# Optimization experiments

Hardware: AMD Instinct MI355X
Metric: run time of the kernel (lower is better)

Reference implementation:

```python
import jax, jax.numpy as jnp
import numpy as np

N_NODES = 100000
N_RAND_EDGES = 1200000
IN_DIM = 64
K = 10  # number of propagation hops


def setup_inputs() -> dict:
    key = jax.random.key(0)
    k1, k2, k3, k4 = jax.random.split(key, 4)
    feats = jax.random.normal(k1, (N_NODES, IN_DIM), dtype=jnp.float32)
    # xavier_uniform with sigmoid gain (=1.0) for s: bound = sqrt(6/(fan_in+fan_out))
    bound = float(np.sqrt(6.0 / (IN_DIM + 1)))
    s = jax.random.uniform(k2, (IN_DIM, 1), dtype=jnp.float32, minval=-bound, maxval=bound)
    src_r = jax.random.randint(k3, (N_RAND_EDGES,), 0, N_NODES)
    dst_r = jax.random.randint(k4, (N_RAND_EDGES,), 0, N_NODES)
    loops = jnp.arange(N_NODES)
    # append self-loops so every node has in_degree >= 1 (finite deg^-0.5)
    src = jnp.concatenate([src_r, loops]).astype(jnp.int64)
    dst = jnp.concatenate([dst_r, loops]).astype(jnp.int64)
    return {"feats": feats, "s": s, "src": src, "dst": dst}


def reference(feats, s, src, dst):
    n = feats.shape[0]
    ones = jnp.ones(src.shape[0], dtype=feats.dtype)
    degs = jax.ops.segment_sum(ones, dst, num_segments=n)  # in-degrees [N]
    norm = (degs ** -0.5)[:, None]  # [N,1]
    results = [feats]
    h = feats
    for _ in range(K):
        h = h * norm                                        # pre-scale
        h = jax.ops.segment_sum(h[src], dst, num_segments=n)  # copy_u + sum SpMM
        h = h * norm                                        # post-scale
        results.append(h)
    H = jnp.stack(results, axis=1)  # [N, K+1, D]
    S = jax.nn.sigmoid(jnp.einsum('nkd,do->nk', H, s))  # [N, K+1] gates
    return jnp.einsum('nk,nkd->nd', S, H)  # [N, D]
```

## Files before the change

### kernel.cpp

```cpp
#include <hip/hip_runtime.h>
#include <hip/hip_bf16.h>
#include <hip/hip_fp16.h>
#include <math.h>


#define DIM 64
#define BSH 9
#define BSZ 512
#define MAXNB 256
#define A2_CHUNK 4096
#define DBINS 64
#define DCHUNK 2048

__global__ void zero_int_kernel(int* __restrict__ p, int n) {
    int i = blockIdx.x * blockDim.x + threadIdx.x;
    if (i < n) p[i] = 0;
}

__global__ void bin_count_kernel(const int* __restrict__ dst,
                                 int* __restrict__ binCount, int E) {
    __shared__ int lb[MAXNB];
    if (threadIdx.x < MAXNB) lb[threadIdx.x] = 0;
    __syncthreads();
    for (int e = blockIdx.x * blockDim.x + threadIdx.x; e < E;
         e += gridDim.x * blockDim.x) {
        atomicAdd(&lb[dst[e] >> BSH], 1);
    }
    __syncthreads();
    if (threadIdx.x < MAXNB && lb[threadIdx.x])
        atomicAdd(&binCount[threadIdx.x], lb[threadIdx.x]);
}

__global__ void binscan_kernel(const int* __restrict__ binCount,
                               int* __restrict__ binBase, int* __restrict__ tail,
                               int* __restrict__ rp, int NB, int N, int E) {
    __shared__ int lds[256];
    int t = threadIdx.x;
    int v = (t < NB) ? binCount[t] : 0;
    lds[t] = v;
    __syncthreads();
    for (int off = 1; off < 256; off <<= 1) {
        int x = (t >= off) ? lds[t - off] : 0;
        __syncthreads();
        lds[t] += x;
        __syncthreads();
    }
    int excl = lds[t] - v;
    if (t < NB) { binBase[t] = excl; tail[t] = excl; }
    if (t == 0) { binBase[NB] = E; rp[N] = E; }
}

__global__ void bin_scatter_kernel(const int* __restrict__ src,
                                   const int* __restrict__ dst,
                                   int* __restrict__ tail,
                                   int2* __restrict__ pairs, int E) {
    __shared__ int cnt[MAXNB];
    __shared__ int base[MAXNB];
    int t = threadIdx.x;
    int begE = blockIdx.x * A2_CHUNK;
    int endE = begE + A2_CHUNK; if (endE > E) endE = E;
    if (t < MAXNB) cnt[t] = 0;
    __syncthreads();
    for (int e = begE + t; e < endE; e += blockDim.x)
        atomicAdd(&cnt[dst[e] >> BSH], 1);
    __syncthreads();
    if (t < MAXNB) {
        int c = cnt[t];
        base[t] = c ? atomicAdd(&tail[t], c) : 0;
        cnt[t] = 0;
    }
    __syncthreads();
    for (int e = begE + t; e < endE; e += blockDim.x) {
        int d = dst[e];
        int b = d >> BSH;
        int pos = base[b] + atomicAdd(&cnt[b], 1);
        pairs[pos] = make_int2(src[e], d);
    }
}

__global__ void bucket_build_kernel(const int2* __restrict__ pairs,
                                    const int* __restrict__ binBase,
                                    int* __restrict__ col, int* __restrict__ rp,
                                    float* __restrict__ norm, int N) {
    __shared__ int degL[BSZ];
    __shared__ int off[BSZ];
    __shared__ int tmp[256];
    int b  = blockIdx.x;
    int lo = b << BSH;
    int cnt = N - lo; if (cnt > BSZ) cnt = BSZ;
    int t = threadIdx.x;
    degL[t] = 0; degL[t + 256] = 0;
    __syncthreads();
    int rbeg = binBase[b], rend = binBase[b + 1];
    for (int j = rbeg + t; j < rend; j += 256)
        atomicAdd(&degL[pairs[j].y - lo], 1);
    __syncthreads();
    int d0 = degL[2 * t], d1 = degL[2 * t + 1];
    int s2 = d0 + d1;
    tmp[t] = s2;
    __syncthreads();
    for (int o = 1; o < 256; o <<= 1) {
        int x = (t >= o) ? tmp[t - o] : 0;
        __syncthreads();
        tmp[t] += x;
        __syncthreads();
    }
    int e2 = tmp[t] - s2;
    off[2 * t]     = e2;
    off[2 * t + 1] = e2 + d0;
    __syncthreads();
    if (2 * t < cnt) {
        rp[lo + 2 * t] = rbeg + e2;
        norm[lo + 2 * t] = rsqrtf((float)d0);
    }
    if (2 * t + 1 < cnt) {
        rp[lo + 2 * t + 1] = rbeg + e2 + d0;
        norm[lo + 2 * t + 1] = rsqrtf((float)d1);
    }
    for (int j = rbeg + t; j < rend; j += 256) {
        int2 p = pairs[j];
        int slot = atomicAdd(&off[p.y - lo], 1);
        col[rbeg + slot] = p.x;
    }
}

__global__ void deg_hist_kernel(const int* __restrict__ rp,
                                int* __restrict__ degCnt, int N) {
    __shared__ int lb[DBINS];
    if (threadIdx.x < DBINS) lb[threadIdx.x] = 0;
    __syncthreads();
    for (int n = blockIdx.x * blockDim.x + threadIdx.x; n < N;
         n += gridDim.x * blockDim.x) {
        int d = rp[n + 1] - rp[n];
        int b = (d < DBINS) ? d : (DBINS - 1);
        atomicAdd(&lb[b], 1);
    }
    __syncthreads();
    if (threadIdx.x < DBINS && lb[threadIdx.x])
        atomicAdd(&degCnt[threadIdx.x], lb[threadIdx.x]);
}

__global__ void deg_scan_kernel(const int* __restrict__ degCnt,
                                int* __restrict__ degCur) {
    __shared__ int lds[DBINS];
    int t = threadIdx.x;
    int rb = DBINS - 1 - t;
    int v = degCnt[rb];
    lds[t] = v;
    __syncthreads();
    for (int off = 1; off < DBINS; off <<= 1) {
        int x = (t >= off) ? lds[t - off] : 0;
        __syncthreads();
        lds[t] += x;
        __syncthreads();
    }
    degCur[rb] = lds[t] - v;
}

__global__ void deg_scatter_kernel(const int* __restrict__ rp,
                                   int* __restrict__ degCur,
                                   int* __restrict__ perm, int N) {
    __shared__ int cnt[DBINS];
    __shared__ int base[DBINS];
    int t = threadIdx.x;
    int beg = blockIdx.x * DCHUNK;
    int endn = beg + DCHUNK; if (endn > N) endn = N;
    if (t < DBINS) cnt[t] = 0;
    __syncthreads();
    for (int n = beg + t; n < endn; n += blockDim.x) {
        int d = rp[n + 1] - rp[n];
        int b = (d < DBINS) ? d : (DBINS - 1);
        atomicAdd(&cnt[b], 1);
    }
    __syncthreads();
    if (t < DBINS) {
        int c = cnt[t];
        base[t] = c ? atomicAdd(&degCur[t], c) : 0;
        cnt[t] = 0;
    }
    __syncthreads();
    for (int n = beg + t; n < endn; n += blockDim.x) {
        int d = rp[n + 1] - rp[n];
        int b = (d < DBINS) ? d : (DBINS - 1);
        int pos = base[b] + atomicAdd(&cnt[b], 1);
        perm[pos] = n;
    }
}

__global__ void init_w0_kernel(const float* __restrict__ feats,
                               const float* __restrict__ norm,
                               __half* __restrict__ w, int N) {
    int n = blockIdx.x * (blockDim.x >> 6) + (threadIdx.x >> 6);
    int lane = threadIdx.x & 63;
    if (n >= N) return;
    size_t idx = ((size_t)n << 6) + lane;
    w[idx] = __float2half(feats[idx] * norm[n]);
}

__global__ void gather_hop_perm_kernel(const __half* __restrict__ w,
                                       const int* __restrict__ rp,
                                       const int* __restrict__ col,
                                       const float* __restrict__ norm,
                                       const int* __restrict__ perm,
                                       __half* __restrict__ wnext, int N) {
    int wid  = (blockIdx.x * blockDim.x + threadIdx.x) >> 6;
    int lane = threadIdx.x & 63;
    int g    = lane >> 3;
    int sub  = lane & 7;
    int gbase = lane & 56;
    int dense = (wid << 3) + g;
    bool valid = (dense < N);
    int n = perm[valid ? dense : (N - 1)];

    int beg = rp[n];
    int end = rp[n + 1];
    int deg = valid ? (end - beg) : 0;
    float nm = norm[n];

    int maxdeg = deg;
    maxdeg = max(maxdeg, __shfl_xor(maxdeg, 8, 64));
    maxdeg = max(maxdeg, __shfl_xor(maxdeg, 16, 64));
    maxdeg = max(maxdeg, __shfl_xor(maxdeg, 32, 64));

    float acc[8];
    #pragma unroll
    for (int i = 0; i < 8; ++i) acc[i] = 0.0f;

    const __half* wsub = w + (sub << 3);

    for (int base = 0; base < maxdeg; base += 8) {
        int i0 = beg + base + sub;
        int c0 = (i0 < end) ? col[i0] : 0;
        #pragma unroll
        for (int jj = 0; jj < 8; ++jj) {
            if (base + jj >= maxdeg) break;
            int cc = __shfl(c0, gbase + jj, 64);
            if (base + jj < deg) {
                float4 raw = *(const float4*)(wsub + ((size_t)cc << 6));
                const __half2* h2 = (const __half2*)&raw;
                float2 f0 = __half22float2(h2[0]);
                float2 f1 = __half22float2(h2[1]);
                float2 f2 = __half22float2(h2[2]);
                float2 f3 = __half22float2(h2[3]);
                acc[0] += f0.x; acc[1] += f0.y;
                acc[2] += f1.x; acc[3] += f1.y;
                acc[4] += f2.x; acc[5] += f2.y;
                acc[6] += f3.x; acc[7] += f3.y;
            }
        }
    }

    if (valid) {
        float n2 = nm * nm;
        __half2 hv[4];
        hv[0] = __floats2half2_rn(acc[0] * n2, acc[1] * n2);
        hv[1] = __floats2half2_rn(acc[2] * n2, acc[3] * n2);
        hv[2] = __floats2half2_rn(acc[4] * n2, acc[5] * n2);
        hv[3] = __floats2half2_rn(acc[6] * n2, acc[7] * n2);
        *(float4*)(wnext + ((size_t)n << 6) + (sub << 3)) = *(const float4*)hv;
    }
}

__global__ void readout_kernel(const __half* __restrict__ wbase,
                               const float* __restrict__ norm,
                               const float* __restrict__ s,
                               float* __restrict__ out,
                               int N, int nk, size_t kstride) {
    int wid  = (blockIdx.x * blockDim.x + threadIdx.x) >> 6;
    int lane = threadIdx.x & 63;
    int g    = lane >> 3;
    int sub  = lane & 7;
    int n    = (wid << 3) + g;
    bool valid = (n < N);
    int nc = valid ? n : (N - 1);

    float4 sa = *(const float4*)(s + (sub << 3));
    float4 sb = *(const float4*)(s + (sub << 3) + 4);

    float inm = 1.0f / norm[nc];
    size_t rowoff = ((size_t)nc << 6) + (sub << 3);

    float acc[8];
    #pragma unroll
    for (int i = 0; i < 8; ++i) acc[i] = 0.0f;

    for (int k = 0; k < nk; ++k) {
        float4 raw = *(const float4*)(wbase + rowoff + (size_t)k * kstride);
        const __half2* h2 = (const __half2*)&raw;
        float2 f0 = __half22float2(h2[0]);
        float2 f1 = __half22float2(h2[1]);
        float2 f2 = __half22float2(h2[2]);
        float2 f3 = __half22float2(h2[3]);
        float p = f0.x * sa.x + f0.y * sa.y + f1.x * sa.z + f1.y * sa.w
                + f2.x * sb.x + f2.y * sb.y + f3.x * sb.z + f3.y * sb.w;
        p += __shfl_xor(p, 1, 64);
        p += __shfl_xor(p, 2, 64);
        p += __shfl_xor(p, 4, 64);
        float gate = 1.0f / (1.0f + expf(-p * inm));
        float g2 = gate * inm;
        acc[0] += g2 * f0.x; acc[1] += g2 * f0.y;
        acc[2] += g2 * f1.x; acc[3] += g2 * f1.y;
        acc[4] += g2 * f2.x; acc[5] += g2 * f2.y;
        acc[6] += g2 * f3.x; acc[7] += g2 * f3.y;
    }

    if (valid) {
        float4 o0 = make_float4(acc[0], acc[1], acc[2], acc[3]);
        float4 o1 = make_float4(acc[4], acc[5], acc[6], acc[7]);
        float4* o = (float4*)(out + rowoff);
        o[0] = o0; o[1] = o1;
    }
}

__global__ void init_kernel(const float* __restrict__ feats,
                            const float* __restrict__ norm,
                            const float* __restrict__ s,
                            float* __restrict__ out,
                            __half* __restrict__ w, int N) {
    int n = blockIdx.x * (blockDim.x >> 6) + (threadIdx.x >> 6);
    int lane = threadIdx.x & 63;
    if (n >= N) return;
    size_t idx = ((size_t)n << 6) + lane;
    float v = feats[idx];
    float p = v * s[lane];
    #pragma unroll
    for (int off = 32; off; off >>= 1) p += __shfl_xor(p, off, 64);
    float gate = 1.0f / (1.0f + expf(-p));
    out[idx] = gate * v;
    w[idx] = __float2half(v * norm[n]);
}

__global__ void gather_hop_kernel(const __half* __restrict__ w,
                                  const int* __restrict__ rp,
                                  const int* __restrict__ col,
                                  const float* __restrict__ norm,
                                  const float* __restrict__ s,
                                  float* __restrict__ out,
                                  __half* __restrict__ wnext,
                                  int N, int write_next) {
    int n = blockIdx.x * (blockDim.x >> 6) + (threadIdx.x >> 6);
    if (n >= N) return;
    int lane = threadIdx.x & 63;
    int e_sub = lane >> 3;
    int c     = lane & 7;

    int beg = rp[n];
    int end = rp[n + 1];

    float acc[8];
    #pragma unroll
    for (int i = 0; i < 8; ++i) acc[i] = 0.0f;

    for (int j = beg + e_sub; j < end; j += 8) {
        int cc = col[j];
        float4 raw = *(const float4*)(w + ((size_t)cc << 6) + (c << 3));
        const __half2* h2 = (const __half2*)&raw;
        float2 f0 = __half22float2(h2[0]);
        float2 f1 = __half22float2(h2[1]);
        float2 f2 = __half22float2(h2[2]);
        float2 f3 = __half22float2(h2[3]);
        acc[0] += f0.x; acc[1] += f0.y;
        acc[2] += f1.x; acc[3] += f1.y;
        acc[4] += f2.x; acc[5] += f2.y;
        acc[6] += f3.x; acc[7] += f3.y;
    }

    #pragma unroll
    for (int off = 8; off < 64; off <<= 1) {
        #pragma unroll
        for (int i = 0; i < 8; ++i) acc[i] += __shfl_xor(acc[i], off, 64);
    }

    float nm = norm[n];
    float v[8];
    #pragma unroll
    for (int i = 0; i < 8; ++i) v[i] = acc[i] * nm;

    float4 sa = *(const float4*)(s + (c << 3));
    float4 sb = *(const float4*)(s + (c << 3) + 4);
    float p = v[0] * sa.x + v[1] * sa.y + v[2] * sa.z + v[3] * sa.w
            + v[4] * sb.x + v[5] * sb.y + v[6] * sb.z + v[7] * sb.w;
    #pragma unroll
    for (int off = 1; off < 8; off <<= 1) p += __shfl_xor(p, off, 64);
    float gate = 1.0f / (1.0f + expf(-p));

    size_t base = ((size_t)n << 6) + (c << 3);
    if (e_sub == 0) {
        float4* o = (float4*)(out + base);
        float4 o0 = o[0], o1 = o[1];
        o0.x += gate * v[0]; o0.y += gate * v[1];
        o0.z += gate * v[2]; o0.w += gate * v[3];
        o1.x += gate * v[4]; o1.y += gate * v[5];
        o1.z += gate * v[6]; o1.w += gate * v[7];
        o[0] = o0; o[1] = o1;
    } else if (e_sub == 1 && write_next) {
        __half2 hv[4];
        hv[0] = __floats2half2_rn(v[0] * nm, v[1] * nm);
        hv[1] = __floats2half2_rn(v[2] * nm, v[3] * nm);
        hv[2] = __floats2half2_rn(v[4] * nm, v[5] * nm);
        hv[3] = __floats2half2_rn(v[6] * nm, v[7] * nm);
        *(float4*)(wnext + base) = *(const float4*)hv;
    }
}

extern "C" void kernel_launch(void* const* d_in, const int* in_sizes, int n_in,
                              void* d_out, int out_size, void* d_ws, size_t ws_size,
                              hipStream_t stream) {
    const float* feats = (const float*)d_in[0];
    const float* s     = (const float*)d_in[1];
    const int*   src   = (const int*)d_in[2];
    const int*   dst   = (const int*)d_in[3];
    float* out = (float*)d_out;

    const int N = in_sizes[0] / DIM;
    const int E = in_sizes[2];
    const int K = 10;
    const int NB = (N + BSZ - 1) >> BSH;

    const int BLK = 256;
    const int wavesPerBlk = BLK / 64;
    int nodeBlocks  = (N + wavesPerBlk - 1) / wavesPerBlk;
    int nodeBlocks8 = (N + wavesPerBlk * 8 - 1) / (wavesPerBlk * 8);
    int a2Blocks  = (E + A2_CHUNK - 1) / A2_CHUNK;
    int dScBlocks = (N + DCHUNK - 1) / DCHUNK;

    size_t stateElems = (size_t)N * DIM;
    size_t intCount = (size_t)(N + 1) + E + 256 + 257 + 256;
    size_t need_full = (size_t)N * 4 + (size_t)(K + 1) * stateElems * 2
                     + intCount * 4 + (size_t)E * 8 + 64;
    int full = (ws_size >= need_full) ? 1 : 0;
    int nbuf = full ? (K + 1) : 2;

    float*  norm    = (float*)d_ws;
    __half* wbase   = (__half*)(norm + N);
    int*    rp      = (int*)(wbase + (size_t)nbuf * stateElems);
    int*    col     = rp + (N + 1);
    int*    binCount= col + E;
    int*    binBase = binCount + 256;
    int*    tail    = binBase + 257;
    size_t  poff    = (size_t)((char*)(tail + 256) - (char*)d_ws);
    poff = (poff + 7) & ~(size_t)7;
    int2*   pairs   = (int2*)((char*)d_ws + poff);
    int*    perm    = (int*)pairs;
    int*    degCnt  = perm + N;
    int*    degCur  = degCnt + DBINS;

    zero_int_kernel<<<1, 256, 0, stream>>>(binCount, 256);
    bin_count_kernel<<<512, BLK, 0, stream>>>(dst, binCount, E);
    binscan_kernel<<<1, 256, 0, stream>>>(binCount, binBase, tail, rp, NB, N, E);
    bin_scatter_kernel<<<a2Blocks, BLK, 0, stream>>>(src, dst, tail, pairs, E);
    bucket_build_kernel<<<NB, 256, 0, stream>>>(pairs, binBase, col, rp, norm, N);

    if (full) {
        zero_int_kernel<<<1, 128, 0, stream>>>(degCnt, 2 * DBINS);
        deg_hist_kernel<<<128, BLK, 0, stream>>>(rp, degCnt, N);
        deg_scan_kernel<<<1, DBINS, 0, stream>>>(degCnt, degCur);
        deg_scatter_kernel<<<dScBlocks, BLK, 0, stream>>>(rp, degCur, perm, N);

        init_w0_kernel<<<nodeBlocks, BLK, 0, stream>>>(feats, norm, wbase, N);
        for (int k = 0; k < K; ++k) {
            const __half* cur = wbase + (size_t)k * stateElems;
            __half* nxt = wbase + (size_t)(k + 1) * stateElems;
            gather_hop_perm_kernel<<<nodeBlocks8, BLK, 0, stream>>>(cur, rp, col,
                                                                    norm, perm,
                                                                    nxt, N);
        }
        readout_kernel<<<nodeBlocks8, BLK, 0, stream>>>(wbase, norm, s, out,
                                                        N, K + 1, stateElems);
    } else {
        __half* wA = wbase;
        __half* wB = wbase + stateElems;
        init_kernel<<<nodeBlocks, BLK, 0, stream>>>(feats, norm, s, out, wA, N);
        __half* cur = wA;
        __half* nxt = wB;
        for (int k = 0; k < K; ++k) {
            int write_next = (k < K - 1) ? 1 : 0;
            gather_hop_kernel<<<nodeBlocks, BLK, 0, stream>>>(cur, rp, col, norm, s,
                                                              out, nxt, N, write_next);
            __half* t = cur; cur = nxt; nxt = t;
        }
    }
}
```

Before: 451.1 us.

## Relabel nodes into degree-sorted order so hop kernels write contiguous rows

Builds an inverse permutation and per-permuted-node begin/end/norm arrays, rewrites column indices into permuted node ids, and stores all hop states in degree-sorted order. Hop writes and readout reads become contiguous, and the perm/rp indirection per node is removed; only the final output is scattered back through perm. The gather loop also issues neighbour loads unconditionally, using clamped indices, to allow more loads in flight. This adds a few setup kernels and one pass over the edges, and it gives up any locality the original node ordering had.

```diff
diff --git a/kernel.cpp b/kernel.cpp
--- a/kernel.cpp
+++ b/kernel.cpp
@@ -187,35 +187,58 @@
     }
 }
 
-__global__ void init_w0_kernel(const float* __restrict__ feats,
-                               const float* __restrict__ norm,
-                               __half* __restrict__ w, int N) {
-    int n = blockIdx.x * (blockDim.x >> 6) + (threadIdx.x >> 6);
+__global__ void perm_meta_kernel(const int* __restrict__ perm,
+                                 const int* __restrict__ rp,
+                                 const float* __restrict__ norm,
+                                 int* __restrict__ begP, int* __restrict__ endP,
+                                 float* __restrict__ normP,
+                                 int* __restrict__ invperm, int N) {
+    int d = blockIdx.x * blockDim.x + threadIdx.x;
+    if (d >= N) return;
+    int n = perm[d];
+    begP[d]  = rp[n];
+    endP[d]  = rp[n + 1];
+    normP[d] = norm[n];
+    invperm[n] = d;
+}
+
+__global__ void col_translate_kernel(int* __restrict__ col,
+                                     const int* __restrict__ invperm, int E) {
+    int j = blockIdx.x * blockDim.x + threadIdx.x;
+    if (j < E) col[j] = invperm[col[j]];
+}
+
+__global__ void init_w0_perm_kernel(const float* __restrict__ feats,
+                                    const float* __restrict__ normP,
+                                    const int* __restrict__ perm,
+                                    __half* __restrict__ w, int N) {
+    int d = blockIdx.x * (blockDim.x >> 6) + (threadIdx.x >> 6);
     int lane = threadIdx.x & 63;
-    if (n >= N) return;
-    size_t idx = ((size_t)n << 6) + lane;
-    w[idx] = __float2half(feats[idx] * norm[n]);
-}
-
-__global__ void gather_hop_perm_kernel(const __half* __restrict__ w,
-                                       const int* __restrict__ rp,
-                                       const int* __restrict__ col,
-                                       const float* __restrict__ norm,
-                                       const int* __restrict__ perm,
-                                       __half* __restrict__ wnext, int N) {
+    if (d >= N) return;
+    int n = perm[d];
+    w[((size_t)d << 6) + lane] =
+        __float2half(feats[((size_t)n << 6) + lane] * normP[d]);
+}
+
+__global__ void gather_hop_dense_kernel(const __half* __restrict__ w,
+                                        const int* __restrict__ begP,
+                                        const int* __restrict__ endP,
+                                        const float* __restrict__ normP,
+                                        const int* __restrict__ col,
+                                        __half* __restrict__ wnext, int N) {
     int wid  = (blockIdx.x * blockDim.x + threadIdx.x) >> 6;
     int lane = threadIdx.x & 63;
     int g    = lane >> 3;
     int sub  = lane & 7;
     int gbase = lane & 56;
-    int dense = (wid << 3) + g;
-    bool valid = (dense < N);
-    int n = perm[valid ? dense : (N - 1)];
-
-    int beg = rp[n];
-    int end = rp[n + 1];
+    int n = (wid << 3) + g;
+    bool valid = (n < N);
+    int nc = valid ? n : (N - 1);
+
+    int beg = begP[nc];
+    int end = endP[nc];
     int deg = valid ? (end - beg) : 0;
-    float nm = norm[n];
+    float nm = normP[nc];
 
     int maxdeg = deg;
     maxdeg = max(maxdeg, __shfl_xor(maxdeg, 8, 64));
@@ -227,16 +250,18 @@
     for (int i = 0; i < 8; ++i) acc[i] = 0.0f;
 
     const __half* wsub = w + (sub << 3);
-
-    for (int base = 0; base < maxdeg; base += 8) {
+    int rounds = (maxdeg + 7) >> 3;
+
+    for (int r = 0; r < rounds; ++r) {
+        int base = r << 3;
         int i0 = beg + base + sub;
-        int c0 = (i0 < end) ? col[i0] : 0;
+        if (i0 >= end) i0 = end - 1;
+        int c0 = col[i0];
         #pragma unroll
         for (int jj = 0; jj < 8; ++jj) {
-            if (base + jj >= maxdeg) break;
             int cc = __shfl(c0, gbase + jj, 64);
+            float4 raw = *(const float4*)(wsub + ((size_t)cc << 6));
             if (base + jj < deg) {
-                float4 raw = *(const float4*)(wsub + ((size_t)cc << 6));
                 const __half2* h2 = (const __half2*)&raw;
                 float2 f0 = __half22float2(h2[0]);
                 float2 f1 = __half22float2(h2[1]);
@@ -261,11 +286,12 @@
     }
 }
 
-__global__ void readout_kernel(const __half* __restrict__ wbase,
-                               const float* __restrict__ norm,
-                               const float* __restrict__ s,
-                               float* __restrict__ out,
-                               int N, int nk, size_t kstride) {
+__global__ void readout_perm_kernel(const __half* __restrict__ wbase,
+                                    const float* __restrict__ normP,
+                                    const int* __restrict__ perm,
+                                    const float* __restrict__ s,
+                                    float* __restrict__ out,
+                                    int N, int nk, size_t kstride) {
     int wid  = (blockIdx.x * blockDim.x + threadIdx.x) >> 6;
     int lane = threadIdx.x & 63;
     int g    = lane >> 3;
@@ -277,7 +303,7 @@
     float4 sa = *(const float4*)(s + (sub << 3));
     float4 sb = *(const float4*)(s + (sub << 3) + 4);
 
-    float inm = 1.0f / norm[nc];
+    float inm = 1.0f / normP[nc];
     size_t rowoff = ((size_t)nc << 6) + (sub << 3);
 
     float acc[8];
@@ -305,9 +331,10 @@
     }
 
     if (valid) {
+        int outn = perm[nc];
         float4 o0 = make_float4(acc[0], acc[1], acc[2], acc[3]);
         float4 o1 = make_float4(acc[4], acc[5], acc[6], acc[7]);
-        float4* o = (float4*)(out + rowoff);
+        float4* o = (float4*)(out + ((size_t)outn << 6) + (sub << 3));
         o[0] = o0; o[1] = o1;
     }
 }
@@ -423,6 +450,8 @@
     int nodeBlocks8 = (N + wavesPerBlk * 8 - 1) / (wavesPerBlk * 8);
     int a2Blocks  = (E + A2_CHUNK - 1) / A2_CHUNK;
     int dScBlocks = (N + DCHUNK - 1) / DCHUNK;
+    int nThrBlocks = (N + BLK - 1) / BLK;
+    int eThrBlocks = (E + BLK - 1) / BLK;
 
     size_t stateElems = (size_t)N * DIM;
     size_t intCount = (size_t)(N + 1) + E + 256 + 257 + 256;
@@ -442,7 +471,11 @@
     poff = (poff + 7) & ~(size_t)7;
     int2*   pairs   = (int2*)((char*)d_ws + poff);
     int*    perm    = (int*)pairs;
-    int*    degCnt  = perm + N;
+    int*    invperm = perm + N;
+    int*    begP    = invperm + N;
+    int*    endP    = begP + N;
+    float*  normP   = (float*)(endP + N);
+    int*    degCnt  = (int*)(normP + N);
     int*    degCur  = degCnt + DBINS;
 
     zero_int_kernel<<<1, 256, 0, stream>>>(binCount, 256);
@@ -456,17 +489,22 @@
         deg_hist_kernel<<<128, BLK, 0, stream>>>(rp, degCnt, N);
         deg_scan_kernel<<<1, DBINS, 0, stream>>>(degCnt, degCur);
         deg_scatter_kernel<<<dScBlocks, BLK, 0, stream>>>(rp, degCur, perm, N);
-
-        init_w0_kernel<<<nodeBlocks, BLK, 0, stream>>>(feats, norm, wbase, N);
+        perm_meta_kernel<<<nThrBlocks, BLK, 0, stream>>>(perm, rp, norm, begP,
+                                                         endP, normP, invperm, N);
+        col_translate_kernel<<<eThrBlocks, BLK, 0, stream>>>(col, invperm, E);
+
+        init_w0_perm_kernel<<<nodeBlocks, BLK, 0, stream>>>(feats, normP, perm,
+                                                            wbase, N);
         for (int k = 0; k < K; ++k) {
             const __half* cur = wbase + (size_t)k * stateElems;
             __half* nxt = wbase + (size_t)(k + 1) * stateElems;
-            gather_hop_perm_kernel<<<nodeBlocks8, BLK, 0, stream>>>(cur, rp, col,
-                                                                    norm, perm,
-                                                                    nxt, N);
+            gather_hop_dense_kernel<<<nodeBlocks8, BLK, 0, stream>>>(cur, begP,
+                                                                     endP, normP,
+                                                                     col, nxt, N);
         }
-        readout_kernel<<<nodeBlocks8, BLK, 0, stream>>>(wbase, norm, s, out,
-                                                        N, K + 1, stateElems);
+        readout_perm_kernel<<<nodeBlocks8, BLK, 0, stream>>>(wbase, normP, perm,
+                                                             s, out, N, K + 1,
+                                                             stateElems);
     } else {
         __half* wA = wbase;
         __half* wB = wbase + stateElems;
```

Result: no change. 458.5 us (+1.6%).
